# Kernel optimization log

Hardware: AMD Instinct MI355X
Metric: run time of the kernel (lower is better)

## Reference

```python
import jax, jax.numpy as jnp
import numpy as np

BASE_NUM = 64
VNUM = 100000
K = 8            # nonzero bases per vertex
NNZ = VNUM * K
DIM = 9
BATCH = 16


def setup_inputs() -> dict:
    key = jax.random.key(0)
    k1, k2, k3 = jax.random.split(key, 3)
    base_fs = jax.random.normal(k1, (BATCH, BASE_NUM * DIM), dtype=jnp.float32)
    ws = jax.random.normal(k2, (NNZ,), dtype=jnp.float32)
    # vv_index: sorted, each vertex appears K times (mirrors mask.T.nonzero())
    vv_index = jnp.repeat(jnp.arange(VNUM, dtype=jnp.int64), K)
    vb_index = jax.random.randint(k3, (NNZ,), 0, BASE_NUM).astype(jnp.int64)
    return {"base_fs": base_fs, "ws": ws, "vb_index": vb_index, "vv_index": vv_index}


def segment_softmax(ws, seg, num_segments):
    m = jax.ops.segment_max(ws, seg, num_segments=num_segments)  # [V]
    e = jnp.exp(ws - m[seg])
    s = jax.ops.segment_sum(e, seg, num_segments=num_segments)   # [V]
    return e / s[seg]


def reference(base_fs, ws, vb_index, vv_index):
    B = base_fs.shape[0]
    w = segment_softmax(ws, vv_index, VNUM)                      # [nnz]
    fs = base_fs.reshape(B, BASE_NUM, DIM)                       # [B, base, dim]
    gathered = fs[:, vb_index, :] * w[None, :, None]             # [B, nnz, dim]
    # scatter-add over the nnz axis into vertices
    v_fs = jax.ops.segment_sum(
        gathered.transpose(1, 0, 2), vv_index, num_segments=VNUM
    )                                                            # [V, B, dim]
    return v_fs.transpose(1, 0, 2)                               # [B, V, dim]
```

## Files before the change

### kernel.cpp

```cpp
#include <hip/hip_runtime.h>

#define BATCH    16
#define BASE_N   64
#define VNUM     100000
#define KNZ      8
#define DIM      9
#define NTHREADS 512
#define WPB      (NTHREADS / 64)
#define VPW      16
#define NTASK    (VNUM / VPW)
#define NBLK     ((NTASK + WPB - 1) / WPB)

__global__ __launch_bounds__(NTHREADS, 4)
void skin_fused(const float* __restrict__ base_fs,
                const float* __restrict__ ws,
                const int*   __restrict__ vb_index,
                float*       __restrict__ out)
{
    __shared__ __align__(16) unsigned short fs_q[BATCH * BASE_N * 8];
    __shared__ float fs_d8[BATCH * BASE_N];
    __shared__ __align__(16) float stage[WPB][8 * 72];

    const int t    = threadIdx.x;
    const int wid  = t >> 6;
    const int lane = t & 63;

    const int  task   = blockIdx.x * WPB + wid;
    const bool active = (task < NTASK);
    const int  v0     = task * VPW;

    float x0 = 0.f, x1 = 0.f;
    int   br0 = 0, br1 = 0;
    if (active) {
        const int g = v0 * KNZ + lane;
        x0 = ws[g];       br0 = vb_index[g];
        x1 = ws[g + 64];  br1 = vb_index[g + 64];
    }

    for (int r = t; r < BATCH * BASE_N; r += NTHREADS) {
        const int b = r >> 6, base = r & 63;
        const float* src = base_fs + r * DIM;
        float v[DIM];
        #pragma unroll
        for (int d = 0; d < DIM; ++d) v[d] = src[d];
        const int qi = (b * 64 + (base ^ (b & 7))) * 8;
        #pragma unroll
        for (int d = 0; d < 8; ++d) {
            unsigned int u = __float_as_uint(v[d]);
            u = (u + 0x7fffu + ((u >> 16) & 1u)) >> 16;
            fs_q[qi + d] = (unsigned short)u;
        }
        fs_d8[b * 64 + (base ^ ((b & 7) << 3))] = v[8];
    }
    __syncthreads();
    if (!active) return;

    const int vloc = lane >> 3;
    const int b0   = lane & 7;
    float* const stg = stage[wid];

    #pragma unroll
    for (int h = 0; h < 2; ++h) {
        const int   vbase = v0 + h * 8;
        const float x     = h ? x1 : x0;
        const int   braw  = h ? br1 : br0;

        float m = x;
        m = fmaxf(m, __shfl_xor(m, 1, 8));
        m = fmaxf(m, __shfl_xor(m, 2, 8));
        m = fmaxf(m, __shfl_xor(m, 4, 8));
        const float e = __expf(x - m);
        float s = e;
        s += __shfl_xor(s, 1, 8);
        s += __shfl_xor(s, 2, 8);
        s += __shfl_xor(s, 4, 8);
        const float w_e = e / s;

        float acc0[DIM], acc1[DIM];
        #pragma unroll
        for (int d = 0; d < DIM; ++d) { acc0[d] = 0.f; acc1[d] = 0.f; }

        #pragma unroll
        for (int k = 0; k < KNZ; ++k) {
            const float wk = __shfl(w_e, k, 8);
            const int   bk = __shfl(braw, k, 8);
            const int sx = (bk ^ b0) << 3;
            const uint4 q0 = *(const uint4*)(fs_q + b0 * 512 + sx);
            const uint4 q1 = *(const uint4*)(fs_q + (b0 + 8) * 512 + sx);
            const int   dx = bk ^ (b0 << 3);
            const float d80 = fs_d8[b0 * 64 + dx];
            const float d81 = fs_d8[(b0 + 8) * 64 + dx];
            float f;
            f = __uint_as_float(q0.x << 16);          acc0[0] = fmaf(wk, f, acc0[0]);
            f = __uint_as_float(q0.x & 0xffff0000u);  acc0[1] = fmaf(wk, f, acc0[1]);
            f = __uint_as_float(q0.y << 16);          acc0[2] = fmaf(wk, f, acc0[2]);
            f = __uint_as_float(q0.y & 0xffff0000u);  acc0[3] = fmaf(wk, f, acc0[3]);
            f = __uint_as_float(q0.z << 16);          acc0[4] = fmaf(wk, f, acc0[4]);
            f = __uint_as_float(q0.z & 0xffff0000u);  acc0[5] = fmaf(wk, f, acc0[5]);
            f = __uint_as_float(q0.w << 16);          acc0[6] = fmaf(wk, f, acc0[6]);
            f = __uint_as_float(q0.w & 0xffff0000u);  acc0[7] = fmaf(wk, f, acc0[7]);
            acc0[8] = fmaf(wk, d80, acc0[8]);
            f = __uint_as_float(q1.x << 16);          acc1[0] = fmaf(wk, f, acc1[0]);
            f = __uint_as_float(q1.x & 0xffff0000u);  acc1[1] = fmaf(wk, f, acc1[1]);
            f = __uint_as_float(q1.y << 16);          acc1[2] = fmaf(wk, f, acc1[2]);
            f = __uint_as_float(q1.y & 0xffff0000u);  acc1[3] = fmaf(wk, f, acc1[3]);
            f = __uint_as_float(q1.z << 16);          acc1[4] = fmaf(wk, f, acc1[4]);
            f = __uint_as_float(q1.z & 0xffff0000u);  acc1[5] = fmaf(wk, f, acc1[5]);
            f = __uint_as_float(q1.w << 16);          acc1[6] = fmaf(wk, f, acc1[6]);
            f = __uint_as_float(q1.w & 0xffff0000u);  acc1[7] = fmaf(wk, f, acc1[7]);
            acc1[8] = fmaf(wk, d81, acc1[8]);
        }

        #pragma unroll
        for (int d = 0; d < DIM; ++d) stg[b0 * 72 + vloc * 9 + d] = acc0[d];
        #pragma unroll
        for (int j = 0; j < 3; ++j) {
            const int i = lane + j * 64;
            if (j < 2 || i < 144) {
                const int b = (int)((unsigned)i / 18u);
                const int f = i - b * 18;
                const float4 val = *(const float4*)(stg + b * 72 + f * 4);
                *(float4*)(out + ((size_t)b * VNUM + vbase) * DIM + f * 4) = val;
            }
        }

        #pragma unroll
        for (int d = 0; d < DIM; ++d) stg[b0 * 72 + vloc * 9 + d] = acc1[d];
        #pragma unroll
        for (int j = 0; j < 3; ++j) {
            const int i = lane + j * 64;
            if (j < 2 || i < 144) {
                const int b = (int)((unsigned)i / 18u);
                const int f = i - b * 18;
                const float4 val = *(const float4*)(stg + b * 72 + f * 4);
                *(float4*)(out + ((size_t)(b + 8) * VNUM + vbase) * DIM + f * 4) = val;
            }
        }
    }
}

extern "C" void kernel_launch(void* const* d_in, const int* in_sizes, int n_in,
                              void* d_out, int out_size, void* d_ws, size_t ws_size,
                              hipStream_t stream) {
    const float* base_fs  = (const float*)d_in[0];
    const float* ws       = (const float*)d_in[1];
    const int*   vb_index = (const int*)d_in[2];
    float* out = (float*)d_out;

    dim3 grid(NBLK), block(NTHREADS);
    hipLaunchKernelGGL(skin_fused, grid, block, 0, stream,
                       base_fs, ws, vb_index, out);
}
```

Measured before the change: 91.17 us.

## Per-lane vectorized softmax loads, paired d8 LDS layout, nontemporal output stores

Each lane now loads all 8 weights and base indices for its vertex with vectorized float4/int4 loads and computes the softmax locally, replacing the 8-lane shuffle reductions and per-k shuffles. The ninth feature column is stored in an interleaved, swizzled LDS layout so that both batch halves come from one float2 read. Output writes use nontemporal stores to avoid polluting cache. The trade-off is redundant global loads (8 lanes read the same vertex data, served by cache), more registers per lane, and the ws/vb_index loads no longer being issued before the LDS staging loop.

After: 96.76 us. 1.06x slower.

```diff
diff --git a/kernel.cpp b/kernel.cpp
--- a/kernel.cpp
+++ b/kernel.cpp
@@ -11,6 +11,8 @@
 #define NTASK    (VNUM / VPW)
 #define NBLK     ((NTASK + WPB - 1) / WPB)
 
+typedef float vfloat4 __attribute__((ext_vector_type(4)));
+
 __global__ __launch_bounds__(NTHREADS, 4)
 void skin_fused(const float* __restrict__ base_fs,
                 const float* __restrict__ ws,
@@ -18,7 +20,7 @@
                 float*       __restrict__ out)
 {
     __shared__ __align__(16) unsigned short fs_q[BATCH * BASE_N * 8];
-    __shared__ float fs_d8[BATCH * BASE_N];
+    __shared__ __align__(8) float fs_d8p[BASE_N * 8 * 2];
     __shared__ __align__(16) float stage[WPB][8 * 72];
 
     const int t    = threadIdx.x;
@@ -28,14 +30,6 @@
     const int  task   = blockIdx.x * WPB + wid;
     const bool active = (task < NTASK);
     const int  v0     = task * VPW;
-
-    float x0 = 0.f, x1 = 0.f;
-    int   br0 = 0, br1 = 0;
-    if (active) {
-        const int g = v0 * KNZ + lane;
-        x0 = ws[g];       br0 = vb_index[g];
-        x1 = ws[g + 64];  br1 = vb_index[g + 64];
-    }
 
     for (int r = t; r < BATCH * BASE_N; r += NTHREADS) {
         const int b = r >> 6, base = r & 63;
@@ -50,7 +44,7 @@
             u = (u + 0x7fffu + ((u >> 16) & 1u)) >> 16;
             fs_q[qi + d] = (unsigned short)u;
         }
-        fs_d8[b * 64 + (base ^ ((b & 7) << 3))] = v[8];
+        fs_d8p[(base * 8 + ((b & 7) ^ (base & 7))) * 2 + (b >> 3)] = v[8];
     }
     __syncthreads();
     if (!active) return;
@@ -61,20 +55,25 @@
 
     #pragma unroll
     for (int h = 0; h < 2; ++h) {
-        const int   vbase = v0 + h * 8;
-        const float x     = h ? x1 : x0;
-        const int   braw  = h ? br1 : br0;
+        const int vbase = v0 + h * 8;
+        const int vme   = vbase + vloc;
 
-        float m = x;
-        m = fmaxf(m, __shfl_xor(m, 1, 8));
-        m = fmaxf(m, __shfl_xor(m, 2, 8));
-        m = fmaxf(m, __shfl_xor(m, 4, 8));
-        const float e = __expf(x - m);
-        float s = e;
-        s += __shfl_xor(s, 1, 8);
-        s += __shfl_xor(s, 2, 8);
-        s += __shfl_xor(s, 4, 8);
-        const float w_e = e / s;
+        const float4 wa = *(const float4*)(ws + (size_t)vme * 8);
+        const float4 wb = *(const float4*)(ws + (size_t)vme * 8 + 4);
+        const int4   ba = *(const int4*)(vb_index + (size_t)vme * 8);
+        const int4   bb = *(const int4*)(vb_index + (size_t)vme * 8 + 4);
+
+        float w[KNZ] = {wa.x, wa.y, wa.z, wa.w, wb.x, wb.y, wb.z, wb.w};
+        const int bs[KNZ] = {ba.x, ba.y, ba.z, ba.w, bb.x, bb.y, bb.z, bb.w};
+
+        float m = fmaxf(fmaxf(fmaxf(w[0], w[1]), fmaxf(w[2], w[3])),
+                        fmaxf(fmaxf(w[4], w[5]), fmaxf(w[6], w[7])));
+        float s = 0.f;
+        #pragma unroll
+        for (int k = 0; k < KNZ; ++k) { w[k] = __expf(w[k] - m); s += w[k]; }
+        const float inv = 1.0f / s;
+        #pragma unroll
+        for (int k = 0; k < KNZ; ++k) w[k] *= inv;
 
         float acc0[DIM], acc1[DIM];
         #pragma unroll
@@ -82,14 +81,12 @@
 
         #pragma unroll
         for (int k = 0; k < KNZ; ++k) {
-            const float wk = __shfl(w_e, k, 8);
-            const int   bk = __shfl(braw, k, 8);
+            const float wk = w[k];
+            const int   bk = bs[k];
             const int sx = (bk ^ b0) << 3;
             const uint4 q0 = *(const uint4*)(fs_q + b0 * 512 + sx);
             const uint4 q1 = *(const uint4*)(fs_q + (b0 + 8) * 512 + sx);
-            const int   dx = bk ^ (b0 << 3);
-            const float d80 = fs_d8[b0 * 64 + dx];
-            const float d81 = fs_d8[(b0 + 8) * 64 + dx];
+            const float2 dp = *(const float2*)(fs_d8p + (bk * 8 + (b0 ^ (bk & 7))) * 2);
             float f;
             f = __uint_as_float(q0.x << 16);          acc0[0] = fmaf(wk, f, acc0[0]);
             f = __uint_as_float(q0.x & 0xffff0000u);  acc0[1] = fmaf(wk, f, acc0[1]);
@@ -99,7 +96,7 @@
             f = __uint_as_float(q0.z & 0xffff0000u);  acc0[5] = fmaf(wk, f, acc0[5]);
             f = __uint_as_float(q0.w << 16);          acc0[6] = fmaf(wk, f, acc0[6]);
             f = __uint_as_float(q0.w & 0xffff0000u);  acc0[7] = fmaf(wk, f, acc0[7]);
-            acc0[8] = fmaf(wk, d80, acc0[8]);
+            acc0[8] = fmaf(wk, dp.x, acc0[8]);
             f = __uint_as_float(q1.x << 16);          acc1[0] = fmaf(wk, f, acc1[0]);
             f = __uint_as_float(q1.x & 0xffff0000u);  acc1[1] = fmaf(wk, f, acc1[1]);
             f = __uint_as_float(q1.y << 16);          acc1[2] = fmaf(wk, f, acc1[2]);
@@ -108,7 +105,7 @@
             f = __uint_as_float(q1.z & 0xffff0000u);  acc1[5] = fmaf(wk, f, acc1[5]);
             f = __uint_as_float(q1.w << 16);          acc1[6] = fmaf(wk, f, acc1[6]);
             f = __uint_as_float(q1.w & 0xffff0000u);  acc1[7] = fmaf(wk, f, acc1[7]);
-            acc1[8] = fmaf(wk, d81, acc1[8]);
+            acc1[8] = fmaf(wk, dp.y, acc1[8]);
         }
 
         #pragma unroll
@@ -119,8 +116,9 @@
             if (j < 2 || i < 144) {
                 const int b = (int)((unsigned)i / 18u);
                 const int f = i - b * 18;
-                const float4 val = *(const float4*)(stg + b * 72 + f * 4);
-                *(float4*)(out + ((size_t)b * VNUM + vbase) * DIM + f * 4) = val;
+                const vfloat4 val = *(const vfloat4*)(stg + b * 72 + f * 4);
+                __builtin_nontemporal_store(
+                    val, (vfloat4*)(out + ((size_t)b * VNUM + vbase) * DIM + f * 4));
             }
         }
 
@@ -132,8 +130,9 @@
             if (j < 2 || i < 144) {
                 const int b = (int)((unsigned)i / 18u);
                 const int f = i - b * 18;
-                const float4 val = *(const float4*)(stg + b * 72 + f * 4);
-                *(float4*)(out + ((size_t)(b + 8) * VNUM + vbase) * DIM + f * 4) = val;
+                const vfloat4 val = *(const vfloat4*)(stg + b * 72 + f * 4);
+                __builtin_nontemporal_store(
+                    val, (vfloat4*)(out + ((size_t)(b + 8) * VNUM + vbase) * DIM + f * 4));
             }
         }
     }
```
